# Kernel optimization log

Hardware: AMD Instinct MI355X
Metric: run time of the kernel (lower is better)

## Reference

```python
import jax, jax.numpy as jnp
import numpy as np

N = 100000   # nodes
E = 800000   # directed edges (before self-loops)
D = 256      # in_feats == out_feats


def setup_inputs() -> dict:
    key = jax.random.key(0)
    ks = jax.random.split(key, 6)
    scale = 1.0 / np.sqrt(D)
    features = jax.random.normal(ks[0], (N, D), dtype=jnp.float32)
    src = jax.random.randint(ks[1], (E,), 0, N, dtype=jnp.int32)
    dst = jax.random.randint(ks[2], (E,), 0, N, dtype=jnp.int32)
    W1 = jax.random.normal(ks[3], (D, D), dtype=jnp.float32) * scale
    b1 = jnp.zeros((D,), dtype=jnp.float32)
    W2 = jax.random.normal(ks[4], (D, D), dtype=jnp.float32) * scale
    b2 = jnp.zeros((D,), dtype=jnp.float32)
    return {"features": features, "src": src, "dst": dst,
            "W1": W1, "b1": b1, "W2": W2, "b2": b2}


def _graph_conv(h, src, dst, norm_src, norm_dst, W, b):
    # DGL GraphConv, norm='both': out = D_in^{-1/2} A (D_out^{-1/2} h W) + b
    h = (h * norm_src) @ W            # [N, D] project (W first; in==out)
    agg = jax.ops.segment_sum(h[src], dst, num_segments=N)  # SpMM gather-scatter
    return agg * norm_dst + b


def reference(features, src, dst, W1, b1, W2, b2):
    # forward does g = dgl.add_self_loop(g)
    loops = jnp.arange(N, dtype=src.dtype)
    s = jnp.concatenate([src, loops])
    d = jnp.concatenate([dst, loops])
    ones = jnp.ones_like(s, dtype=jnp.float32)
    deg_out = jax.ops.segment_sum(ones, s, num_segments=N)   # out-degree (src side)
    deg_in = jax.ops.segment_sum(ones, d, num_segments=N)    # in-degree  (dst side)
    norm_src = jnp.where(deg_out > 0, deg_out ** -0.5, 0.0)[:, None]
    norm_dst = jnp.where(deg_in > 0, deg_in ** -0.5, 0.0)[:, None]
    x = _graph_conv(features, s, d, norm_src, norm_dst, W1, b1)
    x = jax.nn.relu(x)
    x = _graph_conv(x, s, d, norm_src, norm_dst, W2, b2)
    return x
```

## Files before the change

kernel.cpp:

```cpp
#include <hip/hip_runtime.h>

#define NN 100000
#define DD 256
#define SCAN_BLK 1024

typedef unsigned int uint;
typedef unsigned short ushort;
typedef __attribute__((ext_vector_type(8))) short bfx8;
typedef __attribute__((ext_vector_type(4))) float fx4;

__device__ __forceinline__ ushort f2bf(float f) {
    uint u = __float_as_uint(f);
    u += 0x7fff + ((u >> 16) & 1);
    return (ushort)(u >> 16);
}

__device__ __forceinline__ uint cvtpk(float lo, float hi) {
    uint r;
    asm("v_cvt_pk_bf16_f32 %0, %1, %2" : "=v"(r) : "v"(lo), "v"(hi));
    return r;
}

__global__ __launch_bounds__(256) void k_count(const int* __restrict__ src,
                                               const int* __restrict__ dst, int E,
                                               int* __restrict__ dego,
                                               int* __restrict__ degi) {
    int e = blockIdx.x * 256 + threadIdx.x;
    if (e < E) {
        atomicAdd(&dego[src[e]], 1);
        atomicAdd(&degi[dst[e]], 1);
    }
}

__device__ __forceinline__ int block_scan_inc(int v, int* sm) {
    int t = threadIdx.x;
    sm[t] = v;
    __syncthreads();
    for (int o = 1; o < SCAN_BLK; o <<= 1) {
        int x = (t >= o) ? sm[t - o] : 0;
        __syncthreads();
        sm[t] += x;
        __syncthreads();
    }
    return sm[t];
}

__global__ __launch_bounds__(SCAN_BLK) void k_scan1n(const int* __restrict__ degi,
                                                     const int* __restrict__ dego,
                                                     int* __restrict__ partials,
                                                     float* __restrict__ ns,
                                                     float* __restrict__ nd) {
    __shared__ int sm[SCAN_BLK];
    int i = blockIdx.x * SCAN_BLK + threadIdx.x;
    int v = (i < NN) ? degi[i] : 0;
    if (i < NN) {
        ns[i] = rsqrtf((float)(dego[i] + 1));
        nd[i] = rsqrtf((float)(v + 1));
    }
    block_scan_inc(v, sm);
    if (threadIdx.x == 0) partials[blockIdx.x] = sm[SCAN_BLK - 1];
}

__global__ __launch_bounds__(256) void k_scan2cw(int* __restrict__ partials, int nb,
                                                 const float* __restrict__ W1,
                                                 const float* __restrict__ W2,
                                                 ushort* __restrict__ Wf1,
                                                 ushort* __restrict__ Wf2) {
    if (blockIdx.x == 0) {
        __shared__ int sm[128];
        int t = threadIdx.x;
        int v = (t < 128 && t < nb) ? partials[t] : 0;
        if (t < 128) sm[t] = v;
        __syncthreads();
        for (int o = 1; o < 128; o <<= 1) {
            int x = (t < 128 && t >= o) ? sm[t - o] : 0;
            __syncthreads();
            if (t < 128) sm[t] += x;
            __syncthreads();
        }
        if (t < nb) partials[t] = sm[t] - v;
    } else {
        int tid = (blockIdx.x - 1) * 256 + threadIdx.x;
        int m = tid >> 13;
        int r = tid & 8191;
        int lane = r & 63;
        int kf = (r >> 6) & 7;
        int c16 = r >> 9;
        int n = c16 * 16 + (lane & 15);
        int kb = kf * 32 + (lane >> 4) * 8;
        const float* W = m ? W2 : W1;
        ushort* Wf = m ? Wf2 : Wf1;
        uint4 u;
        u.x = (uint)f2bf(W[(size_t)(kb + 0) * DD + n]) |
              ((uint)f2bf(W[(size_t)(kb + 1) * DD + n]) << 16);
        u.y = (uint)f2bf(W[(size_t)(kb + 2) * DD + n]) |
              ((uint)f2bf(W[(size_t)(kb + 3) * DD + n]) << 16);
        u.z = (uint)f2bf(W[(size_t)(kb + 4) * DD + n]) |
              ((uint)f2bf(W[(size_t)(kb + 5) * DD + n]) << 16);
        u.w = (uint)f2bf(W[(size_t)(kb + 6) * DD + n]) |
              ((uint)f2bf(W[(size_t)(kb + 7) * DD + n]) << 16);
        *(uint4*)&Wf[(size_t)r * 8] = u;
    }
}

__global__ __launch_bounds__(SCAN_BLK) void k_scan3(const int* __restrict__ degi,
                                                    const int* __restrict__ partials,
                                                    int* __restrict__ rowptr,
                                                    int* __restrict__ cursor) {
    __shared__ int sm[SCAN_BLK];
    int i = blockIdx.x * SCAN_BLK + threadIdx.x;
    int v = (i < NN) ? degi[i] : 0;
    int incl = block_scan_inc(v, sm);
    int excl = partials[blockIdx.x] + incl - v;
    if (i <= NN) rowptr[i] = excl;
    if (i < NN) cursor[i] = excl;
}

__global__ __launch_bounds__(256) void k_fill(const int* __restrict__ src,
                                              const int* __restrict__ dst, int E,
                                              int* __restrict__ cursor,
                                              int* __restrict__ eidx) {
    int e = blockIdx.x * 256 + threadIdx.x;
    if (e < E) {
        int d = dst[e];
        int p = atomicAdd(&cursor[d], 1);
        eidx[p] = src[e];
    }
}

template <bool FP32A>
__global__ __launch_bounds__(512, 4) void k_mfgemm(const void* __restrict__ Av,
                                                   const float* __restrict__ nrm,
                                                   const ushort* __restrict__ Wf,
                                                   ushort* __restrict__ H) {
    __shared__ uint4 atq[2][128 * 8];
    int t = threadIdx.x;
    int brow = blockIdx.x * 128;
    int lane = t & 63, w = t >> 6;
    int wr = w >> 2, wc = w & 3;
    int lg = lane >> 4, lr = lane & 15;

    int sr = t >> 3, sc = t & 7;
    int rows_[2];
#pragma unroll
    for (int i = 0; i < 2; ++i) {
        int r = brow + sr + i * 64;
        rows_[i] = (r < NN) ? r : NN - 1;
    }
    float4 svf[2][2];
    uint gofs[2];
    if (!FP32A) {
#pragma unroll
        for (int i = 0; i < 2; ++i) {
            int slot = (w * 2 + i) * 64;
            int r = slot / 8 + lane / 8;
            int cs = (lane & 7) ^ (r & 7);
            int row = brow + r;
            if (row >= NN) row = NN - 1;
            gofs[i] = (uint)(((size_t)row * DD + cs * 8) * 2);
        }
    }

    auto ldA = [&](int ks) {
        const float* X = (const float*)Av;
#pragma unroll
        for (int i = 0; i < 2; ++i) {
            const float4* p =
                (const float4*)(X + (size_t)rows_[i] * DD + ks * 64 + sc * 8);
            svf[i][0] = p[0];
            svf[i][1] = p[1];
        }
    };
    auto wrA = [&](int buf) {
#pragma unroll
        for (int i = 0; i < 2; ++i) {
            int r = sr + i * 64;
            uint4 u;
            u.x = cvtpk(svf[i][0].x, svf[i][0].y);
            u.y = cvtpk(svf[i][0].z, svf[i][0].w);
            u.z = cvtpk(svf[i][1].x, svf[i][1].y);
            u.w = cvtpk(svf[i][1].z, svf[i][1].w);
            atq[buf][r * 8 + (sc ^ (r & 7))] = u;
        }
    };
    auto stage = [&](int buf, int ks) {
#pragma unroll
        for (int i = 0; i < 2; ++i) {
            int slot = (w * 2 + i) * 64;
            const char* g = (const char*)Av + gofs[i] + ks * 128;
            __builtin_amdgcn_global_load_lds(
                (const __attribute__((address_space(1))) uint*)g,
                (__attribute__((address_space(3))) uint*)&atq[buf][slot], 16, 0, 0);
        }
    };

    bfx8 bfr2[2][4];
    auto ldB = [&](int ks) {
#pragma unroll
        for (int kk = 0; kk < 2; ++kk)
#pragma unroll
            for (int ni = 0; ni < 4; ++ni)
                bfr2[kk][ni] = *(const bfx8*)&Wf[
                    (((size_t)(wc * 4 + ni) * 8 + (ks * 2 + kk)) * 64 + lane) * 8];
    };

    fx4 acc[4][4];
#pragma unroll
    for (int mi = 0; mi < 4; ++mi)
#pragma unroll
        for (int ni = 0; ni < 4; ++ni)
            acc[mi][ni] = (fx4){0.f, 0.f, 0.f, 0.f};

    if (FP32A) { ldA(0); wrA(0); } else stage(0, 0);
    ldB(0);
    __syncthreads();

    int buf = 0;
#pragma unroll
    for (int ks = 0; ks < 4; ++ks) {
        if (ks < 3) {
            if (FP32A) ldA(ks + 1);
            else stage(buf ^ 1, ks + 1);
        }
#pragma unroll
        for (int kk = 0; kk < 2; ++kk) {
#pragma unroll
            for (int mi = 0; mi < 4; ++mi) {
                int r = wr * 64 + mi * 16 + lr;
                int c = kk * 4 + lg;
                bfx8 af = *(const bfx8*)&atq[buf][r * 8 + (c ^ (r & 7))];
#pragma unroll
                for (int ni = 0; ni < 4; ++ni)
                    acc[mi][ni] = __builtin_amdgcn_mfma_f32_16x16x32_bf16(
                        af, bfr2[kk][ni], acc[mi][ni], 0, 0, 0);
            }
        }
        if (ks < 3) {
            if (FP32A) wrA(buf ^ 1);
            ldB(ks + 1);
        }
        __syncthreads();
        buf ^= 1;
    }

    float scl[4][4];
    if (FP32A) {
#pragma unroll
        for (int mi = 0; mi < 4; ++mi)
#pragma unroll
            for (int j = 0; j < 4; ++j) {
                int row = brow + wr * 64 + mi * 16 + lg * 4 + j;
                scl[mi][j] = nrm[row < NN ? row : NN - 1];
            }
    }
    ushort* hs = (ushort*)&atq[0][0];
#pragma unroll
    for (int h = 0; h < 2; ++h) {
        if (wr == h) {
#pragma unroll
            for (int mi = 0; mi < 4; ++mi)
#pragma unroll
                for (int ni = 0; ni < 4; ++ni)
#pragma unroll
                    for (int j = 0; j < 4; ++j) {
                        int rl = mi * 16 + lg * 4 + j;
                        int c = wc * 64 + ni * 16 + lr;
                        float v = acc[mi][ni][j];
                        if (FP32A) v *= scl[mi][j];
                        hs[rl * 256 + (((c >> 3) ^ (rl & 7)) << 3) + (c & 7)] =
                            f2bf(v);
                    }
        }
        __syncthreads();
        {
            int rl = t >> 3;
            int grow = brow + h * 64 + rl;
            if (grow < NN) {
                ushort* hp = H + (size_t)grow * DD;
#pragma unroll
                for (int i = 0; i < 4; ++i) {
                    int ch = (t & 7) + i * 8;
                    uint4 v = *(const uint4*)&hs[rl * 256 + ((ch ^ (rl & 7)) << 3)];
                    *(uint4*)(hp + ch * 8) = v;
                }
            }
        }
        __syncthreads();
    }
}

__global__ __launch_bounds__(256) void k_spmm_bf(const ushort* __restrict__ T,
                                                 const int* __restrict__ rowptr,
                                                 const int* __restrict__ eidx,
                                                 const float* __restrict__ nd,
                                                 const float* __restrict__ ns,
                                                 const float* __restrict__ bias,
                                                 ushort* __restrict__ obf,
                                                 float* __restrict__ of,
                                                 int layer1) {
    int wid = threadIdx.x >> 6, lane = threadIdx.x & 63;
    int node = blockIdx.x * 4 + wid;
    if (node >= NN) return;
    int c = lane << 2;
    uint2 sv = *(const uint2*)(T + (size_t)node * DD + c);
    float p0[4], p1[4], p2[4], p3[4];
    p0[0] = __uint_as_float(sv.x << 16);
    p0[1] = __uint_as_float(sv.x & 0xffff0000u);
    p0[2] = __uint_as_float(sv.y << 16);
    p0[3] = __uint_as_float(sv.y & 0xffff0000u);
#pragma unroll
    for (int j = 0; j < 4; ++j) { p1[j] = 0.f; p2[j] = 0.f; p3[j] = 0.f; }
    int e = rowptr[node], end = rowptr[node + 1];
    for (; e + 3 < end; e += 4) {
        int s0 = eidx[e], s1 = eidx[e + 1], s2 = eidx[e + 2], s3 = eidx[e + 3];
        uint2 v0 = *(const uint2*)(T + (size_t)s0 * DD + c);
        uint2 v1 = *(const uint2*)(T + (size_t)s1 * DD + c);
        uint2 v2 = *(const uint2*)(T + (size_t)s2 * DD + c);
        uint2 v3 = *(const uint2*)(T + (size_t)s3 * DD + c);
        p0[0] += __uint_as_float(v0.x << 16);
        p0[1] += __uint_as_float(v0.x & 0xffff0000u);
        p0[2] += __uint_as_float(v0.y << 16);
        p0[3] += __uint_as_float(v0.y & 0xffff0000u);
        p1[0] += __uint_as_float(v1.x << 16);
        p1[1] += __uint_as_float(v1.x & 0xffff0000u);
        p1[2] += __uint_as_float(v1.y << 16);
        p1[3] += __uint_as_float(v1.y & 0xffff0000u);
        p2[0] += __uint_as_float(v2.x << 16);
        p2[1] += __uint_as_float(v2.x & 0xffff0000u);
        p2[2] += __uint_as_float(v2.y << 16);
        p2[3] += __uint_as_float(v2.y & 0xffff0000u);
        p3[0] += __uint_as_float(v3.x << 16);
        p3[1] += __uint_as_float(v3.x & 0xffff0000u);
        p3[2] += __uint_as_float(v3.y << 16);
        p3[3] += __uint_as_float(v3.y & 0xffff0000u);
    }
    for (; e < end; ++e) {
        int s0 = eidx[e];
        uint2 v0 = *(const uint2*)(T + (size_t)s0 * DD + c);
        p0[0] += __uint_as_float(v0.x << 16);
        p0[1] += __uint_as_float(v0.x & 0xffff0000u);
        p0[2] += __uint_as_float(v0.y << 16);
        p0[3] += __uint_as_float(v0.y & 0xffff0000u);
    }
#pragma unroll
    for (int j = 0; j < 4; ++j) p0[j] += (p1[j] + p2[j]) + p3[j];
    float n = nd[node];
    float4 bb = *(const float4*)(bias + c);
    float o0 = fmaf(p0[0], n, bb.x);
    float o1 = fmaf(p0[1], n, bb.y);
    float o2 = fmaf(p0[2], n, bb.z);
    float o3 = fmaf(p0[3], n, bb.w);
    if (layer1) {
        float s = ns[node];
        o0 = fmaxf(o0, 0.f) * s; o1 = fmaxf(o1, 0.f) * s;
        o2 = fmaxf(o2, 0.f) * s; o3 = fmaxf(o3, 0.f) * s;
        uint lo = (uint)f2bf(o0) | ((uint)f2bf(o1) << 16);
        uint hi = (uint)f2bf(o2) | ((uint)f2bf(o3) << 16);
        *(uint2*)(obf + (size_t)node * DD + c) = make_uint2(lo, hi);
    } else {
        fx4 o = {o0, o1, o2, o3};
        __builtin_nontemporal_store(o, (fx4*)(of + (size_t)node * DD + c));
    }
}

extern "C" void kernel_launch(void* const* d_in, const int* in_sizes, int n_in,
                              void* d_out, int out_size, void* d_ws, size_t ws_size,
                              hipStream_t stream) {
    const float* features = (const float*)d_in[0];
    const int* src = (const int*)d_in[1];
    const int* dst = (const int*)d_in[2];
    const float* W1 = (const float*)d_in[3];
    const float* b1 = (const float*)d_in[4];
    const float* W2 = (const float*)d_in[5];
    const float* b2 = (const float*)d_in[6];
    int E = in_sizes[1];
    float* out = (float*)d_out;

    size_t off = 0;
    auto alloc = [&](size_t nbytes) -> void* {
        void* p = (char*)d_ws + off;
        off += (nbytes + 255) & ~(size_t)255;
        return p;
    };
    int* dego = (int*)alloc((size_t)NN * 4);
    int* degi = (int*)alloc((size_t)NN * 4);
    float* norm_src = (float*)alloc((size_t)NN * 4);
    float* norm_dst = (float*)alloc((size_t)NN * 4);
    int* rowptr = (int*)alloc((size_t)(NN + 1) * 4);
    int* cursor = (int*)alloc((size_t)NN * 4);
    int* partials = (int*)alloc(128 * 4);
    int* eidx = (int*)alloc((size_t)E * 4);
    ushort* Wf1 = (ushort*)alloc((size_t)DD * DD * 2);
    ushort* Wf2 = (ushort*)alloc((size_t)DD * DD * 2);
    ushort* Xbf = (ushort*)alloc((size_t)NN * DD * 2);
    ushort* Hbf = (ushort*)alloc((size_t)NN * DD * 2);

    const int NB = (NN + SCAN_BLK - 1) / SCAN_BLK;

    hipMemsetAsync(dego, 0, (size_t)2 * 400128, stream);
    k_count<<<(E + 255) / 256, 256, 0, stream>>>(src, dst, E, dego, degi);
    k_scan1n<<<NB, SCAN_BLK, 0, stream>>>(degi, dego, partials, norm_src, norm_dst);
    k_scan2cw<<<65, 256, 0, stream>>>(partials, NB, W1, W2, Wf1, Wf2);
    k_scan3<<<NB, SCAN_BLK, 0, stream>>>(degi, partials, rowptr, cursor);
    k_fill<<<(E + 255) / 256, 256, 0, stream>>>(src, dst, E, cursor, eidx);

    dim3 ggrid((NN + 127) / 128);
    k_mfgemm<true><<<ggrid, 512, 0, stream>>>(features, norm_src, Wf1, Hbf);
    k_spmm_bf<<<(NN + 3) / 4, 256, 0, stream>>>(Hbf, rowptr, eidx, norm_dst,
                                                norm_src, b1, Xbf, out, 1);
    k_mfgemm<false><<<ggrid, 512, 0, stream>>>(Xbf, nullptr, Wf2, Hbf);
    k_spmm_bf<<<(NN + 3) / 4, 256, 0, stream>>>(Hbf, rowptr, eidx, norm_dst,
                                                norm_src, b2, nullptr, out, 0);
}
```

Before: 358.7 us.

## Stage full 128x256 A tile in LDS up front and single-pass epilogue

The GEMM kernel no longer double-buffers K-slices of A with a barrier per slice. It loads the whole 128-row by 256-column bf16 A tile (64KB) into LDS at the start, with fp32 loads interleaved to overlap conversion, then runs all four K steps with no intermediate barriers. The epilogue writes all 128 output rows to LDS in one pass instead of two halves, which removes several syncthreads. The cost is more LDS per block (64KB against 32KB), which may reduce the number of resident blocks per CU and lose overlap between loads and MFMA work.

New measurement: 390.0 us. 1.09x slower.

```diff
diff --git a/kernel.cpp b/kernel.cpp
--- a/kernel.cpp
+++ b/kernel.cpp
@@ -133,66 +133,65 @@
                                                    const float* __restrict__ nrm,
                                                    const ushort* __restrict__ Wf,
                                                    ushort* __restrict__ H) {
-    __shared__ uint4 atq[2][128 * 8];
+    __shared__ uint4 atq[4096];
     int t = threadIdx.x;
     int brow = blockIdx.x * 128;
     int lane = t & 63, w = t >> 6;
     int wr = w >> 2, wc = w & 3;
     int lg = lane >> 4, lr = lane & 15;
 
-    int sr = t >> 3, sc = t & 7;
-    int rows_[2];
-#pragma unroll
-    for (int i = 0; i < 2; ++i) {
-        int r = brow + sr + i * 64;
-        rows_[i] = (r < NN) ? r : NN - 1;
-    }
-    float4 svf[2][2];
-    uint gofs[2];
-    if (!FP32A) {
-#pragma unroll
-        for (int i = 0; i < 2; ++i) {
-            int slot = (w * 2 + i) * 64;
-            int r = slot / 8 + lane / 8;
-            int cs = (lane & 7) ^ (r & 7);
+    if (FP32A) {
+        const float* X = (const float*)Av;
+        float4 sva[2][2], svb[2][2];
+        auto ldF = [&](int b, float4 (*sv)[2]) {
+#pragma unroll
+            for (int s = 0; s < 2; ++s) {
+                int slot = (b * 2 + s) * 512 + t;
+                int ks = slot >> 10, r = (slot & 1023) >> 3;
+                int cc = (slot & 7) ^ (r & 7);
+                int row = brow + r;
+                if (row >= NN) row = NN - 1;
+                const float4* p4 =
+                    (const float4*)(X + (size_t)row * DD + ks * 64 + cc * 8);
+                sv[s][0] = p4[0];
+                sv[s][1] = p4[1];
+            }
+        };
+        auto wrF = [&](int b, const float4 (*sv)[2]) {
+#pragma unroll
+            for (int s = 0; s < 2; ++s) {
+                int slot = (b * 2 + s) * 512 + t;
+                uint4 u;
+                u.x = cvtpk(sv[s][0].x, sv[s][0].y);
+                u.y = cvtpk(sv[s][0].z, sv[s][0].w);
+                u.z = cvtpk(sv[s][1].x, sv[s][1].y);
+                u.w = cvtpk(sv[s][1].z, sv[s][1].w);
+                atq[slot] = u;
+            }
+        };
+        ldF(0, sva);
+        ldF(1, svb);
+        wrF(0, sva);
+        ldF(2, sva);
+        wrF(1, svb);
+        ldF(3, svb);
+        wrF(2, sva);
+        wrF(3, svb);
+    } else {
+#pragma unroll
+        for (int i = 0; i < 8; ++i) {
+            int slot = i * 512 + w * 64 + lane;
+            int ks = slot >> 10, r = (slot & 1023) >> 3;
+            int cs = (slot & 7) ^ (r & 7);
             int row = brow + r;
             if (row >= NN) row = NN - 1;
-            gofs[i] = (uint)(((size_t)row * DD + cs * 8) * 2);
-        }
-    }
-
-    auto ldA = [&](int ks) {
-        const float* X = (const float*)Av;
-#pragma unroll
-        for (int i = 0; i < 2; ++i) {
-            const float4* p =
-                (const float4*)(X + (size_t)rows_[i] * DD + ks * 64 + sc * 8);
-            svf[i][0] = p[0];
-            svf[i][1] = p[1];
-        }
-    };
-    auto wrA = [&](int buf) {
-#pragma unroll
-        for (int i = 0; i < 2; ++i) {
-            int r = sr + i * 64;
-            uint4 u;
-            u.x = cvtpk(svf[i][0].x, svf[i][0].y);
-            u.y = cvtpk(svf[i][0].z, svf[i][0].w);
-            u.z = cvtpk(svf[i][1].x, svf[i][1].y);
-            u.w = cvtpk(svf[i][1].z, svf[i][1].w);
-            atq[buf][r * 8 + (sc ^ (r & 7))] = u;
-        }
-    };
-    auto stage = [&](int buf, int ks) {
-#pragma unroll
-        for (int i = 0; i < 2; ++i) {
-            int slot = (w * 2 + i) * 64;
-            const char* g = (const char*)Av + gofs[i] + ks * 128;
+            const ushort* g = (const ushort*)Av + (size_t)row * DD + ks * 64 + cs * 8;
             __builtin_amdgcn_global_load_lds(
                 (const __attribute__((address_space(1))) uint*)g,
-                (__attribute__((address_space(3))) uint*)&atq[buf][slot], 16, 0, 0);
+                (__attribute__((address_space(3))) uint*)&atq[i * 512 + w * 64],
+                16, 0, 0);
         }
-    };
+    }
 
     bfx8 bfr2[2][4];
     auto ldB = [&](int ks) {
@@ -203,6 +202,7 @@
                 bfr2[kk][ni] = *(const bfx8*)&Wf[
                     (((size_t)(wc * 4 + ni) * 8 + (ks * 2 + kk)) * 64 + lane) * 8];
     };
+    ldB(0);
 
     fx4 acc[4][4];
 #pragma unroll
@@ -211,37 +211,26 @@
         for (int ni = 0; ni < 4; ++ni)
             acc[mi][ni] = (fx4){0.f, 0.f, 0.f, 0.f};
 
-    if (FP32A) { ldA(0); wrA(0); } else stage(0, 0);
-    ldB(0);
     __syncthreads();
 
-    int buf = 0;
 #pragma unroll
     for (int ks = 0; ks < 4; ++ks) {
-        if (ks < 3) {
-            if (FP32A) ldA(ks + 1);
-            else stage(buf ^ 1, ks + 1);
-        }
-#pragma unroll
-        for (int kk = 0; kk < 2; ++kk) {
+#pragma unroll
+        for (int kk = 0; kk < 2; ++kk)
 #pragma unroll
             for (int mi = 0; mi < 4; ++mi) {
                 int r = wr * 64 + mi * 16 + lr;
                 int c = kk * 4 + lg;
-                bfx8 af = *(const bfx8*)&atq[buf][r * 8 + (c ^ (r & 7))];
+                bfx8 af = *(const bfx8*)&atq[ks * 1024 + r * 8 + (c ^ (r & 7))];
 #pragma unroll
                 for (int ni = 0; ni < 4; ++ni)
                     acc[mi][ni] = __builtin_amdgcn_mfma_f32_16x16x32_bf16(
                         af, bfr2[kk][ni], acc[mi][ni], 0, 0, 0);
             }
-        }
-        if (ks < 3) {
-            if (FP32A) wrA(buf ^ 1);
-            ldB(ks + 1);
-        }
-        __syncthreads();
-        buf ^= 1;
-    }
+        if (ks < 3) ldB(ks + 1);
+    }
+
+    __syncthreads();
 
     float scl[4][4];
     if (FP32A) {
@@ -253,39 +242,32 @@
                 scl[mi][j] = nrm[row < NN ? row : NN - 1];
             }
     }
-    ushort* hs = (ushort*)&atq[0][0];
-#pragma unroll
-    for (int h = 0; h < 2; ++h) {
-        if (wr == h) {
-#pragma unroll
-            for (int mi = 0; mi < 4; ++mi)
-#pragma unroll
-                for (int ni = 0; ni < 4; ++ni)
-#pragma unroll
-                    for (int j = 0; j < 4; ++j) {
-                        int rl = mi * 16 + lg * 4 + j;
-                        int c = wc * 64 + ni * 16 + lr;
-                        float v = acc[mi][ni][j];
-                        if (FP32A) v *= scl[mi][j];
-                        hs[rl * 256 + (((c >> 3) ^ (rl & 7)) << 3) + (c & 7)] =
-                            f2bf(v);
-                    }
+    ushort* hs = (ushort*)atq;
+#pragma unroll
+    for (int mi = 0; mi < 4; ++mi)
+#pragma unroll
+        for (int ni = 0; ni < 4; ++ni)
+#pragma unroll
+            for (int j = 0; j < 4; ++j) {
+                int r = wr * 64 + mi * 16 + lg * 4 + j;
+                int c = wc * 64 + ni * 16 + lr;
+                float v = acc[mi][ni][j];
+                if (FP32A) v *= scl[mi][j];
+                hs[r * 256 + (((c >> 3) ^ (r & 7)) << 3) + (c & 7)] = f2bf(v);
+            }
+    __syncthreads();
+    {
+        int rl = t >> 2;
+        int grow = brow + rl;
+        if (grow < NN) {
+            ushort* hp = H + (size_t)grow * DD;
+#pragma unroll
+            for (int i = 0; i < 8; ++i) {
+                int ch = (t & 3) * 8 + i;
+                uint4 v = *(const uint4*)&hs[rl * 256 + ((ch ^ (rl & 7)) << 3)];
+                *(uint4*)(hp + ch * 8) = v;
+            }
         }
-        __syncthreads();
-        {
-            int rl = t >> 3;
-            int grow = brow + h * 64 + rl;
-            if (grow < NN) {
-                ushort* hp = H + (size_t)grow * DD;
-#pragma unroll
-                for (int i = 0; i < 4; ++i) {
-                    int ch = (t & 7) + i * 8;
-                    uint4 v = *(const uint4*)&hs[rl * 256 + ((ch ^ (rl & 7)) << 3)];
-                    *(uint4*)(hp + ch * 8) = v;
-                }
-            }
-        }
-        __syncthreads();
     }
 }
 
```
